# Optimization experiments

Measured on AMD Instinct MI355X. Metric: run time of the kernel, lower is better.

The kernel has to match this reference:

```python
import jax, jax.numpy as jnp
import numpy as np

THRESHOLD = 0.99
B, M, H = 8, 2048, 1024


def setup_inputs():
    key = jax.random.key(0)
    ks = jax.random.split(key, 8)
    x = jax.random.normal(ks[0], (B, M, H), jnp.float32)
    run = jax.random.randint(ks[1], (B, M), 0, 2) > 0
    acc_p = jax.random.uniform(ks[2], (B, M, 1), jnp.float32) * 0.6
    weighted_h = jax.random.normal(ks[3], (B, M, H), jnp.float32)
    remainders = jnp.zeros((B, M, 1), jnp.float32)
    exit_ = jnp.zeros((B, M, 1), jnp.int32)
    pad_h = jax.random.normal(ks[4], (H,), jnp.float32)
    p_w = jax.random.normal(ks[5], (H, 1), jnp.float32) / np.sqrt(H)
    p_b = jnp.zeros((1,), jnp.float32)
    return {"x": x, "run": run, "acc_p": acc_p, "weighted_h": weighted_h,
            "remainders": remainders, "exit_": exit_, "updates": 3,
            "pad_h": pad_h, "p_w": p_w, "p_b": p_b}


def _unpack(x, run):
    # restore left-packed x to full [B, M, H] with zeros at non-run slots
    rank = jnp.cumsum(run, axis=1) - 1                      # [B, M] position in packed row
    g = jnp.take_along_axis(x, jnp.maximum(rank, 0)[..., None], axis=1)
    return jnp.where(run[..., None], g, jnp.zeros((), x.dtype))


def _pack(h, run, pad_h):
    # left-pack run tokens; tail slots get the pad vector (pad_ semantics).
    # Static-shape variant of torch pack: output is [B, M, H] (max_ <= M).
    order = jnp.argsort(~run, axis=1)                       # stable sort: run tokens first
    packed = jnp.take_along_axis(h, order[..., None], axis=1)
    counts = jnp.sum(run, axis=1, keepdims=True)            # [B, 1]
    valid = jnp.arange(run.shape[1])[None, :] < counts      # [B, M]
    return jnp.where(valid[..., None], packed, pad_h[None, None, :])


def reference(x, run, acc_p, weighted_h, remainders, exit_, updates, pad_h, p_w, p_b):
    runf = run[..., None].astype(x.dtype)                   # [B, M, 1]
    h = _unpack(x, run)                                     # [B, M, H]
    p = jax.nn.sigmoid(jnp.einsum('bmh,ho->bmo', h, p_w) + p_b) * runf
    mask_continue = ((acc_p + p) < THRESHOLD) & run[..., None]
    mask_exit = (~mask_continue) & run[..., None]
    mc = mask_continue.astype(x.dtype)
    me = mask_exit.astype(x.dtype)
    update = p * mc + (1.0 - acc_p) * me
    weighted_h_new = h * update + weighted_h
    run_new = run & mask_continue[..., 0]
    acc_p_new = acc_p + update * mc
    remainders_new = remainders + (1.0 - acc_p_new) * me
    updates_new = updates + 1
    exit_new = exit_ + updates_new * mask_exit.astype(exit_.dtype)
    h_packed = _pack(h, run_new, pad_h)
    return (h_packed, weighted_h_new, acc_p_new, remainders_new, run_new, exit_new)
```

## Files before the change

### kernel.cpp

```cpp
#include <hip/hip_runtime.h>

#define BB 8
#define MM 2048
#define HH 1024
#define THRESH 0.99f
#define BMH ((size_t)BB * MM * HH)
#define BM (BB * MM)
#define CHUNK 8
#define NBLK (BM / CHUNK)

typedef float f32x4 __attribute__((ext_vector_type(4)));

__device__ inline f32x4 ntload4(const float* p) {
    return __builtin_nontemporal_load((const f32x4*)p);
}
__device__ inline void ntstore4(float* p, f32x4 v) {
    __builtin_nontemporal_store(v, (f32x4*)p);
}
__device__ inline f32x4 ld4(const float* p) { return *(const f32x4*)p; }

__global__ __launch_bounds__(256, 8) void phase1_kernel(
    const float* __restrict__ x, const int* __restrict__ run,
    const float* __restrict__ acc_p, const float* __restrict__ weighted_h,
    const float* __restrict__ remainders, const int* __restrict__ exit_,
    const int* __restrict__ updates, const float* __restrict__ p_w,
    const float* __restrict__ p_b,
    float* __restrict__ out_wh, float* __restrict__ out_accp,
    float* __restrict__ out_rem, float* __restrict__ out_run,
    float* __restrict__ out_exit, int* __restrict__ run_new_i,
    int* __restrict__ rank_ws) {
    __shared__ int wsum[4];
    __shared__ int cflag[CHUNK];
    __shared__ int crank[CHUNK];

    const int t0 = blockIdx.x * CHUNK;
    const int b  = t0 >> 11;
    const int m0 = t0 & (MM - 1);
    const int* rrow = run + b * MM;
    const int tid  = threadIdx.x;
    const int wave = tid >> 6;
    const int lane = tid & 63;

    int s = 0;
    for (int i = tid; i < m0; i += 256) s += (rrow[i] != 0) ? 1 : 0;
#pragma unroll
    for (int off = 32; off > 0; off >>= 1) s += __shfl_xor(s, off, 64);
    if (lane == 0) wsum[wave] = s;
    if (tid < CHUNK) cflag[tid] = (rrow[m0 + tid] != 0) ? 1 : 0;
    __syncthreads();
    const int base0 = wsum[0] + wsum[1] + wsum[2] + wsum[3];
    if (tid < CHUNK) {
        int r = base0;
#pragma unroll
        for (int i = 0; i < CHUNK; ++i) r += (i <= tid) ? cflag[i] : 0;
        crank[tid] = r - 1;
        rank_ws[t0 + tid] = r - 1;
    }
    __syncthreads();

#pragma unroll
    for (int q = 0; q < 2; ++q) {
        const int ti = wave * 2 + q;
        const int t  = t0 + ti;
        const bool r = (cflag[ti] != 0);
        f32x4 hv[4];
        float dot = 0.f;
        if (r) {
            const float* xrow = x + ((size_t)(b * MM + crank[ti])) * HH;
#pragma unroll
            for (int j = 0; j < 4; ++j) {
                const int idx = j * 256 + lane * 4;
                hv[j] = ld4(xrow + idx);
                const f32x4 wv = ld4(p_w + idx);
                dot += hv[j].x * wv.x + hv[j].y * wv.y +
                       hv[j].z * wv.z + hv[j].w * wv.w;
            }
        } else {
#pragma unroll
            for (int j = 0; j < 4; ++j) hv[j] = (f32x4)(0.f);
        }
#pragma unroll
        for (int off = 32; off > 0; off >>= 1) dot += __shfl_xor(dot, off, 64);

        const float p = r ? (1.f / (1.f + expf(-(dot + p_b[0])))) : 0.f;
        const float ap = acc_p[t];
        const bool mc = r && ((ap + p) < THRESH);
        const bool me = r && !mc;
        const float upd = mc ? p : (me ? (1.f - ap) : 0.f);
        const float ap_new = mc ? (ap + p) : ap;

        const float* whrow = weighted_h + (size_t)t * HH;
        float* orow = out_wh + (size_t)t * HH;
#pragma unroll
        for (int j = 0; j < 4; ++j) {
            const int idx = j * 256 + lane * 4;
            const f32x4 w4 = ntload4(whrow + idx);
            ntstore4(orow + idx, hv[j] * upd + w4);
        }
        if (lane == 0) {
            out_accp[t] = ap_new;
            out_rem[t]  = remainders[t] + (me ? (1.f - ap_new) : 0.f);
            out_run[t]  = mc ? 1.f : 0.f;
            out_exit[t] = (float)(exit_[t] + (me ? (updates[0] + 1) : 0));
            run_new_i[t] = mc ? 1 : 0;
        }
    }
}

__global__ __launch_bounds__(256, 8) void phase2_kernel(
    const float* __restrict__ x, const float* __restrict__ pad_h,
    const int* __restrict__ run_new_i, const int* __restrict__ rank_ws,
    float* __restrict__ h_packed) {
    __shared__ int wsump[4];
    __shared__ int wsuma[4];
    __shared__ int cflag[CHUNK];
    __shared__ int crank2[CHUNK];

    const int t0 = blockIdx.x * CHUNK;
    const int b  = t0 >> 11;
    const int m0 = t0 & (MM - 1);
    const int* nrow = run_new_i + b * MM;
    const int tid  = threadIdx.x;
    const int wave = tid >> 6;
    const int lane = tid & 63;

    int sp = 0, sa = 0;
#pragma unroll
    for (int k = 0; k < MM / 256; ++k) {
        const int i = tid + k * 256;
        const int f = (nrow[i] != 0) ? 1 : 0;
        sa += f;
        if (i < m0) sp += f;
    }
#pragma unroll
    for (int off = 32; off > 0; off >>= 1) {
        sp += __shfl_xor(sp, off, 64);
        sa += __shfl_xor(sa, off, 64);
    }
    if (lane == 0) { wsump[wave] = sp; wsuma[wave] = sa; }
    if (tid < CHUNK) cflag[tid] = (nrow[m0 + tid] != 0) ? 1 : 0;
    __syncthreads();
    const int base0 = wsump[0] + wsump[1] + wsump[2] + wsump[3];
    const int cnt   = wsuma[0] + wsuma[1] + wsuma[2] + wsuma[3];
    if (tid < CHUNK) {
        int r = base0;
#pragma unroll
        for (int i = 0; i < CHUNK; ++i) r += (i <= tid) ? cflag[i] : 0;
        crank2[tid] = r - 1;
    }
    __syncthreads();

#pragma unroll
    for (int q = 0; q < 2; ++q) {
        const int ti = wave * 2 + q;
        const int t  = t0 + ti;
        const int m  = m0 + ti;
        if (cflag[ti] != 0) {
            const float* src = x + ((size_t)(b * MM + rank_ws[t])) * HH;
            float* dst = h_packed + ((size_t)(b * MM + crank2[ti])) * HH;
#pragma unroll
            for (int j = 0; j < 4; ++j) {
                const int idx = j * 256 + lane * 4;
                ntstore4(dst + idx, ld4(src + idx));
            }
        }
        if (m >= cnt) {
            float* prow = h_packed + (size_t)t * HH;
#pragma unroll
            for (int j = 0; j < 4; ++j) {
                const int idx = j * 256 + lane * 4;
                ntstore4(prow + idx, ld4(pad_h + idx));
            }
        }
    }
}

extern "C" void kernel_launch(void* const* d_in, const int* in_sizes, int n_in,
                              void* d_out, int out_size, void* d_ws, size_t ws_size,
                              hipStream_t stream) {
    const float* x          = (const float*)d_in[0];
    const int*   run        = (const int*)d_in[1];
    const float* acc_p      = (const float*)d_in[2];
    const float* weighted_h = (const float*)d_in[3];
    const float* remainders = (const float*)d_in[4];
    const int*   exit_      = (const int*)d_in[5];
    const int*   updates    = (const int*)d_in[6];
    const float* pad_h      = (const float*)d_in[7];
    const float* p_w        = (const float*)d_in[8];
    const float* p_b        = (const float*)d_in[9];

    float* out = (float*)d_out;
    float* out_hpacked = out;
    float* out_wh      = out + BMH;
    float* out_accp    = out + 2 * BMH;
    float* out_rem     = out_accp + BM;
    float* out_run     = out_rem + BM;
    float* out_exit    = out_run + BM;

    int* run_new_i = (int*)d_ws;
    int* rank_ws   = run_new_i + BM;

    phase1_kernel<<<NBLK, 256, 0, stream>>>(x, run, acc_p, weighted_h, remainders,
                                            exit_, updates, p_w, p_b,
                                            out_wh, out_accp, out_rem, out_run,
                                            out_exit, run_new_i, rank_ws);

    phase2_kernel<<<NBLK, 256, 0, stream>>>(x, pad_h, run_new_i, rank_ws,
                                            out_hpacked);
}
```

Before: 48.85 us.

## Split dot/state update from weighted_h update and use chunk bitmasks for pack scan

Phase 1 is split into a small kernel that computes the halting dot products, state outputs, per-token update factors and an 8-bit per-chunk continue mask, and a separate streaming kernel that computes the weighted_h output. The pack kernel computes its prefix counts by popcounting the chunk masks instead of re-scanning the full run_new row. The aim is to shorten the serial dependency and scan overhead, at the cost of re-reading x in the weighted_h kernel and one extra kernel launch.

```diff
diff --git a/kernel.cpp b/kernel.cpp
--- a/kernel.cpp
+++ b/kernel.cpp
@@ -8,6 +8,7 @@
 #define BM (BB * MM)
 #define CHUNK 8
 #define NBLK (BM / CHUNK)
+#define CPR (MM / CHUNK)
 
 typedef float f32x4 __attribute__((ext_vector_type(4)));
 
@@ -19,19 +20,17 @@
 }
 __device__ inline f32x4 ld4(const float* p) { return *(const f32x4*)p; }
 
-__global__ __launch_bounds__(256, 8) void phase1_kernel(
+__global__ __launch_bounds__(256, 8) void kdot(
     const float* __restrict__ x, const int* __restrict__ run,
-    const float* __restrict__ acc_p, const float* __restrict__ weighted_h,
-    const float* __restrict__ remainders, const int* __restrict__ exit_,
-    const int* __restrict__ updates, const float* __restrict__ p_w,
-    const float* __restrict__ p_b,
-    float* __restrict__ out_wh, float* __restrict__ out_accp,
-    float* __restrict__ out_rem, float* __restrict__ out_run,
-    float* __restrict__ out_exit, int* __restrict__ run_new_i,
-    int* __restrict__ rank_ws) {
+    const float* __restrict__ acc_p, const float* __restrict__ remainders,
+    const int* __restrict__ exit_, const int* __restrict__ updates,
+    const float* __restrict__ p_w, const float* __restrict__ p_b,
+    float* __restrict__ out_accp, float* __restrict__ out_rem,
+    float* __restrict__ out_run, float* __restrict__ out_exit,
+    float* __restrict__ upd_ws, int* __restrict__ rank_ws,
+    int* __restrict__ mcmask) {
     __shared__ int wsum[4];
-    __shared__ int cflag[CHUNK];
-    __shared__ int crank[CHUNK];
+    __shared__ int cflag[CHUNK], crank[CHUNK], cnew[CHUNK];
 
     const int t0 = blockIdx.x * CHUNK;
     const int b  = t0 >> 11;
@@ -58,106 +57,117 @@
     }
     __syncthreads();
 
+    const float pb = p_b[0];
+    const int upd1 = updates[0] + 1;
 #pragma unroll
     for (int q = 0; q < 2; ++q) {
         const int ti = wave * 2 + q;
         const int t  = t0 + ti;
         const bool r = (cflag[ti] != 0);
-        f32x4 hv[4];
         float dot = 0.f;
         if (r) {
             const float* xrow = x + ((size_t)(b * MM + crank[ti])) * HH;
 #pragma unroll
             for (int j = 0; j < 4; ++j) {
                 const int idx = j * 256 + lane * 4;
-                hv[j] = ld4(xrow + idx);
+                const f32x4 hv = ld4(xrow + idx);
                 const f32x4 wv = ld4(p_w + idx);
-                dot += hv[j].x * wv.x + hv[j].y * wv.y +
-                       hv[j].z * wv.z + hv[j].w * wv.w;
+                dot += hv.x * wv.x + hv.y * wv.y + hv.z * wv.z + hv.w * wv.w;
             }
-        } else {
-#pragma unroll
-            for (int j = 0; j < 4; ++j) hv[j] = (f32x4)(0.f);
         }
 #pragma unroll
         for (int off = 32; off > 0; off >>= 1) dot += __shfl_xor(dot, off, 64);
 
-        const float p = r ? (1.f / (1.f + expf(-(dot + p_b[0])))) : 0.f;
-        const float ap = acc_p[t];
-        const bool mc = r && ((ap + p) < THRESH);
-        const bool me = r && !mc;
-        const float upd = mc ? p : (me ? (1.f - ap) : 0.f);
-        const float ap_new = mc ? (ap + p) : ap;
-
+        if (lane == 0) {
+            const float p = r ? (1.f / (1.f + expf(-(dot + pb)))) : 0.f;
+            const float ap = acc_p[t];
+            const bool mc = r && ((ap + p) < THRESH);
+            const bool me = r && !mc;
+            const float upd = mc ? p : (me ? (1.f - ap) : 0.f);
+            const float ap_new = mc ? (ap + p) : ap;
+            out_accp[t] = ap_new;
+            out_rem[t]  = remainders[t] + (me ? (1.f - ap_new) : 0.f);
+            out_run[t]  = mc ? 1.f : 0.f;
+            out_exit[t] = (float)(exit_[t] + (me ? upd1 : 0));
+            upd_ws[t]   = upd;
+            cnew[ti]    = mc ? 1 : 0;
+        }
+    }
+    __syncthreads();
+    if (tid == 0) {
+        int m16 = 0;
+#pragma unroll
+        for (int i = 0; i < CHUNK; ++i) m16 |= cnew[i] << i;
+        mcmask[blockIdx.x] = m16;
+    }
+}
+
+__global__ __launch_bounds__(256, 8) void kwh(
+    const float* __restrict__ x, const int* __restrict__ run,
+    const float* __restrict__ weighted_h, const float* __restrict__ upd_ws,
+    const int* __restrict__ rank_ws, float* __restrict__ out_wh) {
+    const int t0 = blockIdx.x * CHUNK;
+    const int b  = t0 >> 11;
+    const int wave = threadIdx.x >> 6;
+    const int lane = threadIdx.x & 63;
+
+#pragma unroll
+    for (int q = 0; q < 2; ++q) {
+        const int ti = wave * 2 + q;
+        const int t  = t0 + ti;
+        const bool r = (run[t] != 0);
+        const float upd = upd_ws[t];
+        const float* xrow = x + ((size_t)(b * MM + rank_ws[t])) * HH;
         const float* whrow = weighted_h + (size_t)t * HH;
         float* orow = out_wh + (size_t)t * HH;
 #pragma unroll
         for (int j = 0; j < 4; ++j) {
             const int idx = j * 256 + lane * 4;
             const f32x4 w4 = ntload4(whrow + idx);
-            ntstore4(orow + idx, hv[j] * upd + w4);
-        }
-        if (lane == 0) {
-            out_accp[t] = ap_new;
-            out_rem[t]  = remainders[t] + (me ? (1.f - ap_new) : 0.f);
-            out_run[t]  = mc ? 1.f : 0.f;
-            out_exit[t] = (float)(exit_[t] + (me ? (updates[0] + 1) : 0));
-            run_new_i[t] = mc ? 1 : 0;
-        }
-    }
-}
-
-__global__ __launch_bounds__(256, 8) void phase2_kernel(
+            f32x4 hv = (f32x4)(0.f);
+            if (r) hv = ld4(xrow + idx);
+            ntstore4(orow + idx, hv * upd + w4);
+        }
+    }
+}
+
+__global__ __launch_bounds__(256, 8) void kpack(
     const float* __restrict__ x, const float* __restrict__ pad_h,
-    const int* __restrict__ run_new_i, const int* __restrict__ rank_ws,
+    const int* __restrict__ mcmask, const int* __restrict__ rank_ws,
     float* __restrict__ h_packed) {
-    __shared__ int wsump[4];
-    __shared__ int wsuma[4];
-    __shared__ int cflag[CHUNK];
-    __shared__ int crank2[CHUNK];
-
-    const int t0 = blockIdx.x * CHUNK;
-    const int b  = t0 >> 11;
-    const int m0 = t0 & (MM - 1);
-    const int* nrow = run_new_i + b * MM;
+    __shared__ int wsump[4], wsuma[4];
+
+    const int t0  = blockIdx.x * CHUNK;
+    const int b   = t0 >> 11;
+    const int m0  = t0 & (MM - 1);
+    const int myc = blockIdx.x & (CPR - 1);
     const int tid  = threadIdx.x;
     const int wave = tid >> 6;
     const int lane = tid & 63;
 
-    int sp = 0, sa = 0;
-#pragma unroll
-    for (int k = 0; k < MM / 256; ++k) {
-        const int i = tid + k * 256;
-        const int f = (nrow[i] != 0) ? 1 : 0;
-        sa += f;
-        if (i < m0) sp += f;
-    }
+    const int pc = __popc(mcmask[b * CPR + tid] & 0xFF);
+    int sp = (tid < myc) ? pc : 0;
+    int sa = pc;
 #pragma unroll
     for (int off = 32; off > 0; off >>= 1) {
         sp += __shfl_xor(sp, off, 64);
         sa += __shfl_xor(sa, off, 64);
     }
     if (lane == 0) { wsump[wave] = sp; wsuma[wave] = sa; }
-    if (tid < CHUNK) cflag[tid] = (nrow[m0 + tid] != 0) ? 1 : 0;
-    __syncthreads();
-    const int base0 = wsump[0] + wsump[1] + wsump[2] + wsump[3];
+    __syncthreads();
+    const int baseN = wsump[0] + wsump[1] + wsump[2] + wsump[3];
     const int cnt   = wsuma[0] + wsuma[1] + wsuma[2] + wsuma[3];
-    if (tid < CHUNK) {
-        int r = base0;
-#pragma unroll
-        for (int i = 0; i < CHUNK; ++i) r += (i <= tid) ? cflag[i] : 0;
-        crank2[tid] = r - 1;
-    }
-    __syncthreads();
+    const int mybits = mcmask[blockIdx.x] & 0xFF;
 
 #pragma unroll
     for (int q = 0; q < 2; ++q) {
         const int ti = wave * 2 + q;
         const int t  = t0 + ti;
         const int m  = m0 + ti;
-        if (cflag[ti] != 0) {
+        if ((mybits >> ti) & 1) {
+            const int dstrow = baseN + __popc(mybits & ((1 << (ti + 1)) - 1)) - 1;
             const float* src = x + ((size_t)(b * MM + rank_ws[t])) * HH;
-            float* dst = h_packed + ((size_t)(b * MM + crank2[ti])) * HH;
+            float* dst = h_packed + ((size_t)(b * MM + dstrow)) * HH;
 #pragma unroll
             for (int j = 0; j < 4; ++j) {
                 const int idx = j * 256 + lane * 4;
@@ -197,14 +207,15 @@
     float* out_run     = out_rem + BM;
     float* out_exit    = out_run + BM;
 
-    int* run_new_i = (int*)d_ws;
-    int* rank_ws   = run_new_i + BM;
-
-    phase1_kernel<<<NBLK, 256, 0, stream>>>(x, run, acc_p, weighted_h, remainders,
-                                            exit_, updates, p_w, p_b,
-                                            out_wh, out_accp, out_rem, out_run,
-                                            out_exit, run_new_i, rank_ws);
-
-    phase2_kernel<<<NBLK, 256, 0, stream>>>(x, pad_h, run_new_i, rank_ws,
-                                            out_hpacked);
-}
+    float* upd_ws  = (float*)d_ws;
+    int*   rank_ws = (int*)(upd_ws + BM);
+    int*   mc_ws   = rank_ws + BM;
+
+    kdot<<<NBLK, 256, 0, stream>>>(x, run, acc_p, remainders, exit_, updates,
+                                   p_w, p_b, out_accp, out_rem, out_run,
+                                   out_exit, upd_ws, rank_ws, mc_ws);
+
+    kwh<<<NBLK, 256, 0, stream>>>(x, run, weighted_h, upd_ws, rank_ws, out_wh);
+
+    kpack<<<NBLK, 256, 0, stream>>>(x, pad_h, mc_ws, rank_ws, out_hpacked);
+}
```

Result: slower. 53.67 us (+9.9%).

## Compact run_new into per-chunk bitmasks and vectorize phase1 prefix count

Applied to the files above, without the earlier changes.

Phase1 now writes one 8-bit mask per chunk of eight tokens instead of a per-token int run_new array. Phase2 computes its prefix and total counts from 256 popcounts per row rather than rescanning 2048 ints. Phase1's prefix count over the run row switches to int4 vector loads. This cuts the redundant per-block scanning of the row in both kernels, at the cost of an extra block-wide barrier in phase1.

```diff
diff --git a/kernel.cpp b/kernel.cpp
--- a/kernel.cpp
+++ b/kernel.cpp
@@ -8,6 +8,7 @@
 #define BM (BB * MM)
 #define CHUNK 8
 #define NBLK (BM / CHUNK)
+#define CPR (MM / CHUNK)
 
 typedef float f32x4 __attribute__((ext_vector_type(4)));
 
@@ -27,11 +28,12 @@
     const float* __restrict__ p_b,
     float* __restrict__ out_wh, float* __restrict__ out_accp,
     float* __restrict__ out_rem, float* __restrict__ out_run,
-    float* __restrict__ out_exit, int* __restrict__ run_new_i,
+    float* __restrict__ out_exit, int* __restrict__ mcmask,
     int* __restrict__ rank_ws) {
     __shared__ int wsum[4];
     __shared__ int cflag[CHUNK];
     __shared__ int crank[CHUNK];
+    __shared__ int cnew[CHUNK];
 
     const int t0 = blockIdx.x * CHUNK;
     const int b  = t0 >> 11;
@@ -42,7 +44,12 @@
     const int lane = tid & 63;
 
     int s = 0;
-    for (int i = tid; i < m0; i += 256) s += (rrow[i] != 0) ? 1 : 0;
+    const int n4 = m0 >> 2;
+    const int4* rrow4 = (const int4*)rrow;
+    for (int i = tid; i < n4; i += 256) {
+        const int4 v = rrow4[i];
+        s += (v.x != 0) + (v.y != 0) + (v.z != 0) + (v.w != 0);
+    }
 #pragma unroll
     for (int off = 32; off > 0; off >>= 1) s += __shfl_xor(s, off, 64);
     if (lane == 0) wsum[wave] = s;
@@ -102,62 +109,56 @@
             out_rem[t]  = remainders[t] + (me ? (1.f - ap_new) : 0.f);
             out_run[t]  = mc ? 1.f : 0.f;
             out_exit[t] = (float)(exit_[t] + (me ? (updates[0] + 1) : 0));
-            run_new_i[t] = mc ? 1 : 0;
-        }
+            cnew[ti] = mc ? 1 : 0;
+        }
+    }
+    __syncthreads();
+    if (tid == 0) {
+        int m8 = 0;
+#pragma unroll
+        for (int i = 0; i < CHUNK; ++i) m8 |= cnew[i] << i;
+        mcmask[blockIdx.x] = m8;
     }
 }
 
 __global__ __launch_bounds__(256, 8) void phase2_kernel(
     const float* __restrict__ x, const float* __restrict__ pad_h,
-    const int* __restrict__ run_new_i, const int* __restrict__ rank_ws,
+    const int* __restrict__ mcmask, const int* __restrict__ rank_ws,
     float* __restrict__ h_packed) {
-    __shared__ int wsump[4];
-    __shared__ int wsuma[4];
-    __shared__ int cflag[CHUNK];
-    __shared__ int crank2[CHUNK];
-
-    const int t0 = blockIdx.x * CHUNK;
-    const int b  = t0 >> 11;
-    const int m0 = t0 & (MM - 1);
-    const int* nrow = run_new_i + b * MM;
+    __shared__ int wsump[4], wsuma[4];
+
+    const int t0  = blockIdx.x * CHUNK;
+    const int b   = t0 >> 11;
+    const int m0  = t0 & (MM - 1);
+    const int myc = blockIdx.x & (CPR - 1);
     const int tid  = threadIdx.x;
     const int wave = tid >> 6;
     const int lane = tid & 63;
 
-    int sp = 0, sa = 0;
-#pragma unroll
-    for (int k = 0; k < MM / 256; ++k) {
-        const int i = tid + k * 256;
-        const int f = (nrow[i] != 0) ? 1 : 0;
-        sa += f;
-        if (i < m0) sp += f;
-    }
+    const int mymask = mcmask[b * CPR + tid] & 0xFF;
+    const int pc = __popc(mymask);
+    int sp = (tid < myc) ? pc : 0;
+    int sa = pc;
 #pragma unroll
     for (int off = 32; off > 0; off >>= 1) {
         sp += __shfl_xor(sp, off, 64);
         sa += __shfl_xor(sa, off, 64);
     }
     if (lane == 0) { wsump[wave] = sp; wsuma[wave] = sa; }
-    if (tid < CHUNK) cflag[tid] = (nrow[m0 + tid] != 0) ? 1 : 0;
-    __syncthreads();
-    const int base0 = wsump[0] + wsump[1] + wsump[2] + wsump[3];
+    __syncthreads();
+    const int baseN = wsump[0] + wsump[1] + wsump[2] + wsump[3];
     const int cnt   = wsuma[0] + wsuma[1] + wsuma[2] + wsuma[3];
-    if (tid < CHUNK) {
-        int r = base0;
-#pragma unroll
-        for (int i = 0; i < CHUNK; ++i) r += (i <= tid) ? cflag[i] : 0;
-        crank2[tid] = r - 1;
-    }
-    __syncthreads();
+    const int mybits = mcmask[blockIdx.x] & 0xFF;
 
 #pragma unroll
     for (int q = 0; q < 2; ++q) {
         const int ti = wave * 2 + q;
         const int t  = t0 + ti;
         const int m  = m0 + ti;
-        if (cflag[ti] != 0) {
+        if ((mybits >> ti) & 1) {
+            const int dstrow = baseN + __popc(mybits & ((1 << (ti + 1)) - 1)) - 1;
             const float* src = x + ((size_t)(b * MM + rank_ws[t])) * HH;
-            float* dst = h_packed + ((size_t)(b * MM + crank2[ti])) * HH;
+            float* dst = h_packed + ((size_t)(b * MM + dstrow)) * HH;
 #pragma unroll
             for (int j = 0; j < 4; ++j) {
                 const int idx = j * 256 + lane * 4;
@@ -197,14 +198,14 @@
     float* out_run     = out_rem + BM;
     float* out_exit    = out_run + BM;
 
-    int* run_new_i = (int*)d_ws;
-    int* rank_ws   = run_new_i + BM;
+    int* mcmask  = (int*)d_ws;
+    int* rank_ws = mcmask + NBLK;
 
     phase1_kernel<<<NBLK, 256, 0, stream>>>(x, run, acc_p, weighted_h, remainders,
                                             exit_, updates, p_w, p_b,
                                             out_wh, out_accp, out_rem, out_run,
-                                            out_exit, run_new_i, rank_ws);
-
-    phase2_kernel<<<NBLK, 256, 0, stream>>>(x, pad_h, run_new_i, rank_ws,
+                                            out_exit, mcmask, rank_ws);
+
+    phase2_kernel<<<NBLK, 256, 0, stream>>>(x, pad_h, mcmask, rank_ws,
                                             out_hpacked);
 }
```

Measured after the change: 46.68 us. -4.4%, faster.
